# Kernel optimization log

Hardware: AMD Instinct MI355X
Metric: run time of the kernel (lower is better)

## Reference

```python
import jax, jax.numpy as jnp
import numpy as np

NSLICES = 4
HID = 512
IN_FEAT = 342   # input_shape - 1 (last column is phase)
OUT = 311
BATCH = 256


def cubic(y0, y1, y2, y3, mu):
    # Catmull-Rom cubic interpolation, as in the original PFNN code
    return (
        (-0.5 * y0 + 1.5 * y1 - 1.5 * y2 + 0.5 * y3) * mu * mu * mu
        + (y0 - 2.5 * y1 + 2.0 * y2 - 0.5 * y3) * mu * mu
        + (-0.5 * y0 + 0.5 * y2) * mu
        + y1
    )


def setup_inputs() -> dict:
    key = jax.random.key(0)
    ks = jax.random.split(key, 7)
    x = jax.random.uniform(ks[0], (BATCH, IN_FEAT + 1), dtype=jnp.float32)
    s = 0.02
    W0 = jax.random.normal(ks[1], (NSLICES, HID, IN_FEAT), dtype=jnp.float32) * s
    b0 = jax.random.normal(ks[2], (NSLICES, HID), dtype=jnp.float32) * s
    W1 = jax.random.normal(ks[3], (NSLICES, HID, HID), dtype=jnp.float32) * s
    b1 = jax.random.normal(ks[4], (NSLICES, HID), dtype=jnp.float32) * s
    W2 = jax.random.normal(ks[5], (NSLICES, OUT, HID), dtype=jnp.float32) * s
    b2 = jax.random.normal(ks[6], (NSLICES, OUT), dtype=jnp.float32) * s
    return {"x": x, "W0": W0, "b0": b0, "W1": W1, "b1": b1, "W2": W2, "b2": b2}


def reference(x, W0, b0, W1, b1, W2, b2):
    phase = x[:, -1]                       # [B]
    pscale = NSLICES * phase
    mu = jnp.mod(pscale, 1.0)              # [B]
    i1 = jnp.floor(pscale).astype(jnp.int32) % NSLICES
    i0 = (i1 - 1) % NSLICES
    i2 = (i1 + 1) % NSLICES
    i3 = (i1 + 2) % NSLICES
    muW = mu[:, None, None]                # broadcast over (out, in)
    mub = mu[:, None]

    Wb0 = cubic(W0[i0], W0[i1], W0[i2], W0[i3], muW)   # [B, 512, 342]
    bb0 = cubic(b0[i0], b0[i1], b0[i2], b0[i3], mub)   # [B, 512]
    Wb1 = cubic(W1[i0], W1[i1], W1[i2], W1[i3], muW)   # [B, 512, 512]
    bb1 = cubic(b1[i0], b1[i1], b1[i2], b1[i3], mub)
    Wb2 = cubic(W2[i0], W2[i1], W2[i2], W2[i3], muW)   # [B, 311, 512]
    bb2 = cubic(b2[i0], b2[i1], b2[i2], b2[i3], mub)

    h = x[:, :-1]                                       # [B, 342]
    h = jax.nn.elu(jnp.einsum('boi,bi->bo', Wb0, h) + bb0)
    h = jax.nn.elu(jnp.einsum('boi,bi->bo', Wb1, h) + bb1)
    out = jnp.einsum('boi,bi->bo', Wb2, h) + bb2        # [B, 311]
    return out
```

## Files before the change

### kernel.cpp

```cpp
#include <hip/hip_runtime.h>
#include <math.h>

#define HID 512
#define IN_FEAT 342
#define OUTD 311
#define BATCH 256
#define KP0 352
#define XROW (IN_FEAT + 1)
#define NB 32
#define NTHR 512

#define NT0 32
#define NCC0 11
#define NT1 32
#define NCC1 16
#define NT2 20
#define NCC2 16

#define P0 (4 * 512 * 44)
#define P1 (4 * 512 * 64)
#define P2 (4 * 320 * 64)
#define PTOT (P0 + P1 + P2)

typedef unsigned short u16;
typedef short bf16x8 __attribute__((ext_vector_type(8)));
typedef float f32x4 __attribute__((ext_vector_type(4)));

__device__ __forceinline__ u16 f2bf_rne(float v) {
    unsigned int x = __float_as_uint(v);
    unsigned int r = (x + 0x7fffu + ((x >> 16) & 1u)) >> 16;
    return (u16)r;
}
__device__ __forceinline__ float bf2f(u16 u) {
    return __uint_as_float(((unsigned int)u) << 16);
}

union U8 { u16 u[8]; uint4 v; };

__device__ __forceinline__ void split8(const float* __restrict__ src, bf16x8& hi, bf16x8& lo) {
#pragma unroll
    for (int j = 0; j < 8; j++) {
        u16 h = f2bf_rne(src[j]);
        hi[j] = (short)h;
        lo[j] = (short)f2bf_rne(src[j] - bf2f(h));
    }
}

__global__ __launch_bounds__(256) void prep_frag(
    const float* __restrict__ W0, const float* __restrict__ W1, const float* __restrict__ W2,
    u16* __restrict__ F0, u16* __restrict__ F1, u16* __restrict__ F2)
{
    int i = blockIdx.x * 256 + threadIdx.x;
    if (i >= PTOT) return;

    float src[8];
    u16* dst;
    if (i < P0) {
        int s = i / (512 * 44);
        int rem = i - s * (512 * 44);
        int row = rem / 44, c = rem - row * 44;
        int k = c * 8;
        const float* rp = W0 + ((size_t)s * 512 + row) * IN_FEAT;
        if (k + 8 <= IN_FEAT) {
            const float2* p2 = reinterpret_cast<const float2*>(rp + k);
            float2 v0 = p2[0], v1 = p2[1], v2 = p2[2], v3 = p2[3];
            src[0] = v0.x; src[1] = v0.y; src[2] = v1.x; src[3] = v1.y;
            src[4] = v2.x; src[5] = v2.y; src[6] = v3.x; src[7] = v3.y;
        } else {
#pragma unroll
            for (int j = 0; j < 8; j++) src[j] = (k + j < IN_FEAT) ? rp[k + j] : 0.f;
        }
        int ot = row >> 4, m = row & 15, cc = c >> 2, q = c & 3;
        dst = F0 + ((size_t)(s * NT0 + ot) * NCC0 + cc) * 1024 + (q * 16 + m) * 8;
    } else if (i < P0 + P1) {
        int l = i - P0;
        int s = l >> 15;
        int row = (l >> 6) & 511, c = l & 63;
        int k = c * 8;
        const float4* p4 = reinterpret_cast<const float4*>(
            W1 + ((size_t)s * 512 + row) * 512 + k);
        float4 v0 = p4[0], v1 = p4[1];
        src[0] = v0.x; src[1] = v0.y; src[2] = v0.z; src[3] = v0.w;
        src[4] = v1.x; src[5] = v1.y; src[6] = v1.z; src[7] = v1.w;
        int ot = row >> 4, m = row & 15, cc = c >> 2, q = c & 3;
        dst = F1 + ((size_t)(s * NT1 + ot) * NCC1 + cc) * 1024 + (q * 16 + m) * 8;
    } else {
        int l = i - P0 - P1;
        int s = l / (320 * 64);
        int rem = l - s * (320 * 64);
        int row = rem >> 6, c = rem & 63;
        int k = c * 8;
        if (row < OUTD) {
            const float4* p4 = reinterpret_cast<const float4*>(
                W2 + ((size_t)s * OUTD + row) * 512 + k);
            float4 v0 = p4[0], v1 = p4[1];
            src[0] = v0.x; src[1] = v0.y; src[2] = v0.z; src[3] = v0.w;
            src[4] = v1.x; src[5] = v1.y; src[6] = v1.z; src[7] = v1.w;
        } else {
#pragma unroll
            for (int j = 0; j < 8; j++) src[j] = 0.f;
        }
        int ot = row >> 4, m = row & 15, cc = c >> 2, q = c & 3;
        dst = F2 + ((size_t)(s * NT2 + ot) * NCC2 + cc) * 1024 + (q * 16 + m) * 8;
    }

    U8 hi, lo;
#pragma unroll
    for (int j = 0; j < 8; j++) {
        u16 h = f2bf_rne(src[j]);
        hi.u[j] = h;
        lo.u[j] = f2bf_rne(src[j] - bf2f(h));
    }
    *reinterpret_cast<uint4*>(dst)       = hi.v;
    *reinterpret_cast<uint4*>(dst + 512) = lo.v;
}

template<int KP, int KLDS, int FINAL, int MODE, int NT, int NBY>
__global__ __launch_bounds__(NTHR, 1) void layer_frag(
    const u16* __restrict__ Wf, const float* __restrict__ x,
    const u16* __restrict__ Hhi, const u16* __restrict__ Hlo,
    const float* __restrict__ bias, int Mb,
    u16* __restrict__ Ohi, u16* __restrict__ Olo, float* __restrict__ outp)
{
    union SharedU {
        u16 h[2][NB * KLDS];
        float acc[4][NB][17];
    };
    __shared__ SharedU sm;

    const int blk = (int)blockIdx.x;
    const int bx = (blk >> 3) & 7;
    const int by = (blk & 7) | ((blk >> 6) << 3);
    if (by >= NBY) return;

    const int tid = (int)threadIdx.x;
    const int b0 = bx * NB;
    const int o0 = by * 16;

    constexpr int CH = KP / 8;
    if constexpr (MODE == 0) {
        for (int idx = tid; idx < NB * CH; idx += NTHR) {
            int r = idx / CH, c = idx - r * CH;
            int k = c * 8;
            const float* xr = x + (size_t)(b0 + r) * XROW;
            float src[8];
#pragma unroll
            for (int j = 0; j < 8; j++) {
                int kk = k + j;
                src[j] = (kk < IN_FEAT) ? xr[kk] : 0.f;
            }
            bf16x8 hi, lo;
            split8(src, hi, lo);
            *reinterpret_cast<bf16x8*>(&sm.h[0][r * KLDS + k]) = hi;
            *reinterpret_cast<bf16x8*>(&sm.h[1][r * KLDS + k]) = lo;
        }
    } else {
        for (int idx = tid; idx < NB * CH; idx += NTHR) {
            int r = idx / CH, c = idx - r * CH;
            size_t g = (size_t)(b0 + r) * KP + c * 8;
            *reinterpret_cast<uint4*>(&sm.h[0][r * KLDS + c * 8]) =
                *reinterpret_cast<const uint4*>(Hhi + g);
            *reinterpret_cast<uint4*>(&sm.h[1][r * KLDS + c * 8]) =
                *reinterpret_cast<const uint4*>(Hlo + g);
        }
    }
    __syncthreads();

    const int lane = tid & 63;
    const int w = tid >> 6;
    const int s = w & 3;
    const int t = w >> 2;
    const int m = lane & 15;
    const int q = lane >> 4;

    constexpr int NCC = KP / 32;
    const u16* wf = Wf + ((size_t)(s * NT + by) * NCC) * 1024 + lane * 8;
    const u16* hp  = &sm.h[0][(t * 16 + m) * KLDS + q * 8];
    const u16* hpl = &sm.h[1][(t * 16 + m) * KLDS + q * 8];

    const int brow = b0 + t * 16 + m;
    const float ps = 4.f * x[(size_t)brow * XROW + IN_FEAT];
    const float fl = floorf(ps);
    const float mu = ps - fl;
    const int i1 = ((int)fl) & 3;
    const int jj = (s - i1) & 3;
    const float mu2 = mu * mu, mu3 = mu2 * mu;
    const float ds = (jj == 0) ? ( 1.5f * mu3 - 2.5f * mu2 + 1.0f)
                   : (jj == 1) ? (-1.5f * mu3 + 2.0f * mu2 + 0.5f * mu)
                   : (jj == 2) ? ( 0.5f * mu3 - 0.5f * mu2)
                   :             (-0.5f * mu3 + mu2 - 0.5f * mu);

    f32x4 a0 = {0.f, 0.f, 0.f, 0.f};
    f32x4 a1 = {0.f, 0.f, 0.f, 0.f};
    f32x4 a2 = {0.f, 0.f, 0.f, 0.f};
#pragma unroll
    for (int cc = 0; cc < NCC; ++cc) {
        bf16x8 ah = *reinterpret_cast<const bf16x8*>(wf + cc * 1024);
        bf16x8 al = *reinterpret_cast<const bf16x8*>(wf + cc * 1024 + 512);
        bf16x8 bh = *reinterpret_cast<const bf16x8*>(hp + cc * 32);
        bf16x8 bl = *reinterpret_cast<const bf16x8*>(hpl + cc * 32);
        a0 = __builtin_amdgcn_mfma_f32_16x16x32_bf16(ah, bh, a0, 0, 0, 0);
        a1 = __builtin_amdgcn_mfma_f32_16x16x32_bf16(ah, bl, a1, 0, 0, 0);
        a2 = __builtin_amdgcn_mfma_f32_16x16x32_bf16(al, bh, a2, 0, 0, 0);
    }
    __syncthreads();

    f32x4 sum = a0 + a1 + a2;
#pragma unroll
    for (int r = 0; r < 4; ++r) {
        int o = o0 + q * 4 + r;
        float bb = (o < Mb) ? bias[(size_t)s * Mb + o] : 0.f;
        sm.acc[s][t * 16 + m][q * 4 + r] = ds * (sum[r] + bb);
    }
    __syncthreads();

    const int b_l = tid >> 4;
    const int o_l = tid & 15;
    float vv = sm.acc[0][b_l][o_l] + sm.acc[1][b_l][o_l]
             + sm.acc[2][b_l][o_l] + sm.acc[3][b_l][o_l];
    const int o = o0 + o_l;
    const int b = b0 + b_l;
    if (!FINAL) {
        float e = (vv > 0.f) ? vv : expm1f(vv);
        u16 h = f2bf_rne(e);
        Ohi[(size_t)b * HID + o] = h;
        Olo[(size_t)b * HID + o] = f2bf_rne(e - bf2f(h));
    } else if (o < OUTD) {
        outp[(size_t)b * OUTD + o] = vv;
    }
}

extern "C" void kernel_launch(void* const* d_in, const int* in_sizes, int n_in,
                              void* d_out, int out_size, void* d_ws, size_t ws_size,
                              hipStream_t stream) {
    const float* x  = (const float*)d_in[0];
    const float* W0 = (const float*)d_in[1];
    const float* b0v = (const float*)d_in[2];
    const float* W1 = (const float*)d_in[3];
    const float* b1v = (const float*)d_in[4];
    const float* W2 = (const float*)d_in[5];
    const float* b2v = (const float*)d_in[6];
    float* out = (float*)d_out;

    char* pw = (char*)d_ws;
    auto alloc = [&](size_t bytes) { char* r = pw; pw += (bytes + 255) & ~(size_t)255; return r; };

    u16* F0 = (u16*)alloc((size_t)4 * NT0 * NCC0 * 1024 * 2);
    u16* F1 = (u16*)alloc((size_t)4 * NT1 * NCC1 * 1024 * 2);
    u16* F2 = (u16*)alloc((size_t)4 * NT2 * NCC2 * 1024 * 2);
    u16* hahi = (u16*)alloc((size_t)BATCH * HID * 2);
    u16* halo = (u16*)alloc((size_t)BATCH * HID * 2);
    u16* hbhi = (u16*)alloc((size_t)BATCH * HID * 2);
    u16* hblo = (u16*)alloc((size_t)BATCH * HID * 2);

    prep_frag<<<PTOT / 256, 256, 0, stream>>>(W0, W1, W2, F0, F1, F2);

    layer_frag<KP0, 360, 0, 0, NT0, 32><<<256, NTHR, 0, stream>>>(
        F0, x, nullptr, nullptr, b0v, HID, hahi, halo, nullptr);

    layer_frag<HID, 520, 0, 1, NT1, 32><<<256, NTHR, 0, stream>>>(
        F1, x, hahi, halo, b1v, HID, hbhi, hblo, nullptr);

    layer_frag<HID, 520, 1, 1, NT2, 20><<<192, NTHR, 0, stream>>>(
        F2, x, hbhi, hblo, b2v, OUTD, nullptr, nullptr, out);
}
```

Measured before the change: 99.91 us.

## Stage weight fragments through LDS in prep and halve batch tile per block

The weight preprocessing kernel now gives each block one 16-row output tile. It converts the tile to hi/lo bf16 in shared memory, then writes it out as contiguous uint4 stores instead of scattered 16-byte writes. The layer kernels drop from 32 to 16 batch rows and from 512 to 256 threads per block, doubling the grid and allowing up to 4 blocks per CU. The aim is to coalesce global writes in prep and improve occupancy and latency hiding in the GEMV-like layers. In exchange, each weight fragment is reloaded from global memory twice as often across batch tiles.

```diff
diff --git a/kernel.cpp b/kernel.cpp
--- a/kernel.cpp
+++ b/kernel.cpp
@@ -7,8 +7,8 @@
 #define BATCH 256
 #define KP0 352
 #define XROW (IN_FEAT + 1)
-#define NB 32
-#define NTHR 512
+#define NB 16
+#define NTHR 256
 
 #define NT0 32
 #define NCC0 11
@@ -17,11 +17,6 @@
 #define NT2 20
 #define NCC2 16
 
-#define P0 (4 * 512 * 44)
-#define P1 (4 * 512 * 64)
-#define P2 (4 * 320 * 64)
-#define PTOT (P0 + P1 + P2)
-
 typedef unsigned short u16;
 typedef short bf16x8 __attribute__((ext_vector_type(8)));
 typedef float f32x4 __attribute__((ext_vector_type(4)));
@@ -50,73 +45,99 @@
     const float* __restrict__ W0, const float* __restrict__ W1, const float* __restrict__ W2,
     u16* __restrict__ F0, u16* __restrict__ F1, u16* __restrict__ F2)
 {
-    int i = blockIdx.x * 256 + threadIdx.x;
-    if (i >= PTOT) return;
-
-    float src[8];
-    u16* dst;
-    if (i < P0) {
-        int s = i / (512 * 44);
-        int rem = i - s * (512 * 44);
-        int row = rem / 44, c = rem - row * 44;
-        int k = c * 8;
-        const float* rp = W0 + ((size_t)s * 512 + row) * IN_FEAT;
-        if (k + 8 <= IN_FEAT) {
-            const float2* p2 = reinterpret_cast<const float2*>(rp + k);
-            float2 v0 = p2[0], v1 = p2[1], v2 = p2[2], v3 = p2[3];
-            src[0] = v0.x; src[1] = v0.y; src[2] = v1.x; src[3] = v1.y;
-            src[4] = v2.x; src[5] = v2.y; src[6] = v3.x; src[7] = v3.y;
-        } else {
-#pragma unroll
-            for (int j = 0; j < 8; j++) src[j] = (k + j < IN_FEAT) ? rp[k + j] : 0.f;
-        }
-        int ot = row >> 4, m = row & 15, cc = c >> 2, q = c & 3;
-        dst = F0 + ((size_t)(s * NT0 + ot) * NCC0 + cc) * 1024 + (q * 16 + m) * 8;
-    } else if (i < P0 + P1) {
-        int l = i - P0;
-        int s = l >> 15;
-        int row = (l >> 6) & 511, c = l & 63;
-        int k = c * 8;
-        const float4* p4 = reinterpret_cast<const float4*>(
-            W1 + ((size_t)s * 512 + row) * 512 + k);
-        float4 v0 = p4[0], v1 = p4[1];
-        src[0] = v0.x; src[1] = v0.y; src[2] = v0.z; src[3] = v0.w;
-        src[4] = v1.x; src[5] = v1.y; src[6] = v1.z; src[7] = v1.w;
-        int ot = row >> 4, m = row & 15, cc = c >> 2, q = c & 3;
-        dst = F1 + ((size_t)(s * NT1 + ot) * NCC1 + cc) * 1024 + (q * 16 + m) * 8;
+    __shared__ u16 fr[16 * 1024];
+    const int bid = (int)blockIdx.x;
+    const int tid = (int)threadIdx.x;
+
+    if (bid < 128) {
+        const int s = bid >> 5, ot = bid & 31;
+        for (int idx = tid; idx < 16 * 44; idx += 256) {
+            int rr = idx / 44, c = idx - rr * 44;
+            int k = c * 8;
+            const float* rp = W0 + (size_t)(s * 512 + ot * 16 + rr) * IN_FEAT;
+            float src[8];
+            if (k + 8 <= IN_FEAT) {
+                const float2* p2 = reinterpret_cast<const float2*>(rp + k);
+                float2 v0 = p2[0], v1 = p2[1], v2 = p2[2], v3 = p2[3];
+                src[0] = v0.x; src[1] = v0.y; src[2] = v1.x; src[3] = v1.y;
+                src[4] = v2.x; src[5] = v2.y; src[6] = v3.x; src[7] = v3.y;
+            } else {
+#pragma unroll
+                for (int j = 0; j < 8; j++) src[j] = (k + j < IN_FEAT) ? rp[k + j] : 0.f;
+            }
+            U8 hi, lo;
+#pragma unroll
+            for (int j = 0; j < 8; j++) {
+                u16 h = f2bf_rne(src[j]);
+                hi.u[j] = h;
+                lo.u[j] = f2bf_rne(src[j] - bf2f(h));
+            }
+            int cc = c >> 2, lane = (c & 3) * 16 + rr;
+            *reinterpret_cast<uint4*>(&fr[cc * 1024 + lane * 8])       = hi.v;
+            *reinterpret_cast<uint4*>(&fr[cc * 1024 + 512 + lane * 8]) = lo.v;
+        }
+        __syncthreads();
+        uint4* dst = reinterpret_cast<uint4*>(F0 + (size_t)(s * NT0 + ot) * NCC0 * 1024);
+        const uint4* srcp = reinterpret_cast<const uint4*>(fr);
+        for (int idx = tid; idx < NCC0 * 128; idx += 256) dst[idx] = srcp[idx];
+    } else if (bid < 256) {
+        const int l = bid - 128;
+        const int s = l >> 5, ot = l & 31;
+        for (int idx = tid; idx < 16 * 64; idx += 256) {
+            int rr = idx >> 6, c = idx & 63;
+            const float4* p4 = reinterpret_cast<const float4*>(
+                W1 + (size_t)(s * 512 + ot * 16 + rr) * 512 + c * 8);
+            float4 v0 = p4[0], v1 = p4[1];
+            float src[8] = {v0.x, v0.y, v0.z, v0.w, v1.x, v1.y, v1.z, v1.w};
+            U8 hi, lo;
+#pragma unroll
+            for (int j = 0; j < 8; j++) {
+                u16 h = f2bf_rne(src[j]);
+                hi.u[j] = h;
+                lo.u[j] = f2bf_rne(src[j] - bf2f(h));
+            }
+            int cc = c >> 2, lane = (c & 3) * 16 + rr;
+            *reinterpret_cast<uint4*>(&fr[cc * 1024 + lane * 8])       = hi.v;
+            *reinterpret_cast<uint4*>(&fr[cc * 1024 + 512 + lane * 8]) = lo.v;
+        }
+        __syncthreads();
+        uint4* dst = reinterpret_cast<uint4*>(F1 + (size_t)(s * NT1 + ot) * NCC1 * 1024);
+        const uint4* srcp = reinterpret_cast<const uint4*>(fr);
+        for (int idx = tid; idx < NCC1 * 128; idx += 256) dst[idx] = srcp[idx];
     } else {
-        int l = i - P0 - P1;
-        int s = l / (320 * 64);
-        int rem = l - s * (320 * 64);
-        int row = rem >> 6, c = rem & 63;
-        int k = c * 8;
-        if (row < OUTD) {
-            const float4* p4 = reinterpret_cast<const float4*>(
-                W2 + ((size_t)s * OUTD + row) * 512 + k);
-            float4 v0 = p4[0], v1 = p4[1];
-            src[0] = v0.x; src[1] = v0.y; src[2] = v0.z; src[3] = v0.w;
-            src[4] = v1.x; src[5] = v1.y; src[6] = v1.z; src[7] = v1.w;
-        } else {
-#pragma unroll
-            for (int j = 0; j < 8; j++) src[j] = 0.f;
-        }
-        int ot = row >> 4, m = row & 15, cc = c >> 2, q = c & 3;
-        dst = F2 + ((size_t)(s * NT2 + ot) * NCC2 + cc) * 1024 + (q * 16 + m) * 8;
-    }
-
-    U8 hi, lo;
-#pragma unroll
-    for (int j = 0; j < 8; j++) {
-        u16 h = f2bf_rne(src[j]);
-        hi.u[j] = h;
-        lo.u[j] = f2bf_rne(src[j] - bf2f(h));
-    }
-    *reinterpret_cast<uint4*>(dst)       = hi.v;
-    *reinterpret_cast<uint4*>(dst + 512) = lo.v;
+        const int l = bid - 256;
+        const int s = l / 20, ot = l - s * 20;
+        for (int idx = tid; idx < 16 * 64; idx += 256) {
+            int rr = idx >> 6, c = idx & 63;
+            int orow = ot * 16 + rr;
+            float src[8] = {0.f, 0.f, 0.f, 0.f, 0.f, 0.f, 0.f, 0.f};
+            if (orow < OUTD) {
+                const float4* p4 = reinterpret_cast<const float4*>(
+                    W2 + ((size_t)s * OUTD + orow) * 512 + c * 8);
+                float4 v0 = p4[0], v1 = p4[1];
+                src[0] = v0.x; src[1] = v0.y; src[2] = v0.z; src[3] = v0.w;
+                src[4] = v1.x; src[5] = v1.y; src[6] = v1.z; src[7] = v1.w;
+            }
+            U8 hi, lo;
+#pragma unroll
+            for (int j = 0; j < 8; j++) {
+                u16 h = f2bf_rne(src[j]);
+                hi.u[j] = h;
+                lo.u[j] = f2bf_rne(src[j] - bf2f(h));
+            }
+            int cc = c >> 2, lane = (c & 3) * 16 + rr;
+            *reinterpret_cast<uint4*>(&fr[cc * 1024 + lane * 8])       = hi.v;
+            *reinterpret_cast<uint4*>(&fr[cc * 1024 + 512 + lane * 8]) = lo.v;
+        }
+        __syncthreads();
+        uint4* dst = reinterpret_cast<uint4*>(F2 + (size_t)(s * NT2 + ot) * NCC2 * 1024);
+        const uint4* srcp = reinterpret_cast<const uint4*>(fr);
+        for (int idx = tid; idx < NCC2 * 128; idx += 256) dst[idx] = srcp[idx];
+    }
 }
 
 template<int KP, int KLDS, int FINAL, int MODE, int NT, int NBY>
-__global__ __launch_bounds__(NTHR, 1) void layer_frag(
+__global__ __launch_bounds__(NTHR, 4) void layer_frag(
     const u16* __restrict__ Wf, const float* __restrict__ x,
     const u16* __restrict__ Hhi, const u16* __restrict__ Hlo,
     const float* __restrict__ bias, int Mb,
@@ -129,8 +150,8 @@
     __shared__ SharedU sm;
 
     const int blk = (int)blockIdx.x;
-    const int bx = (blk >> 3) & 7;
-    const int by = (blk & 7) | ((blk >> 6) << 3);
+    const int bx = (blk >> 3) & 15;
+    const int by = (blk & 7) | ((blk >> 7) << 3);
     if (by >= NBY) return;
 
     const int tid = (int)threadIdx.x;
@@ -167,18 +188,16 @@
     __syncthreads();
 
     const int lane = tid & 63;
-    const int w = tid >> 6;
-    const int s = w & 3;
-    const int t = w >> 2;
+    const int s = tid >> 6;
     const int m = lane & 15;
     const int q = lane >> 4;
 
     constexpr int NCC = KP / 32;
     const u16* wf = Wf + ((size_t)(s * NT + by) * NCC) * 1024 + lane * 8;
-    const u16* hp  = &sm.h[0][(t * 16 + m) * KLDS + q * 8];
-    const u16* hpl = &sm.h[1][(t * 16 + m) * KLDS + q * 8];
-
-    const int brow = b0 + t * 16 + m;
+    const u16* hp  = &sm.h[0][m * KLDS + q * 8];
+    const u16* hpl = &sm.h[1][m * KLDS + q * 8];
+
+    const int brow = b0 + m;
     const float ps = 4.f * x[(size_t)brow * XROW + IN_FEAT];
     const float fl = floorf(ps);
     const float mu = ps - fl;
@@ -210,7 +229,7 @@
     for (int r = 0; r < 4; ++r) {
         int o = o0 + q * 4 + r;
         float bb = (o < Mb) ? bias[(size_t)s * Mb + o] : 0.f;
-        sm.acc[s][t * 16 + m][q * 4 + r] = ds * (sum[r] + bb);
+        sm.acc[s][m][q * 4 + r] = ds * (sum[r] + bb);
     }
     __syncthreads();
 
@@ -253,14 +272,14 @@
     u16* hbhi = (u16*)alloc((size_t)BATCH * HID * 2);
     u16* hblo = (u16*)alloc((size_t)BATCH * HID * 2);
 
-    prep_frag<<<PTOT / 256, 256, 0, stream>>>(W0, W1, W2, F0, F1, F2);
-
-    layer_frag<KP0, 360, 0, 0, NT0, 32><<<256, NTHR, 0, stream>>>(
+    prep_frag<<<336, 256, 0, stream>>>(W0, W1, W2, F0, F1, F2);
+
+    layer_frag<KP0, 360, 0, 0, NT0, 32><<<512, NTHR, 0, stream>>>(
         F0, x, nullptr, nullptr, b0v, HID, hahi, halo, nullptr);
 
-    layer_frag<HID, 520, 0, 1, NT1, 32><<<256, NTHR, 0, stream>>>(
+    layer_frag<HID, 520, 0, 1, NT1, 32><<<512, NTHR, 0, stream>>>(
         F1, x, hahi, halo, b1v, HID, hbhi, hblo, nullptr);
 
-    layer_frag<HID, 520, 1, 1, NT2, 20><<<192, NTHR, 0, stream>>>(
+    layer_frag<HID, 520, 1, 1, NT2, 20><<<384, NTHR, 0, stream>>>(
         F2, x, hbhi, hblo, b2v, OUTD, nullptr, nullptr, out);
 }
```

Result: no change. 99.56 us (-0.3%).
